# Optimization experiments

Measured on AMD Instinct MI355X. Metric: run time of the kernel, lower is better.

The kernel has to match this reference:

```python
import jax, jax.numpy as jnp
import numpy as np

N = 50000      # nodes
E = 600000     # edges
D_IN = 128     # node_dim
D = 128        # out_channels
T = 4          # num_node_types
R = 4          # num_edge_types
L = 2          # num_layers
C = 8          # num_class
G = 512        # graphs in batch


def setup_inputs() -> dict:
    key = jax.random.key(0)
    ks = jax.random.split(key, 12)
    s = 0.05
    x = jax.random.normal(ks[0], (N, D_IN), jnp.float32)
    node_type = jax.random.randint(ks[1], (N,), 0, T)
    edge_index = jax.random.randint(ks[2], (2, E), 0, N)
    edge_type = jax.random.randint(ks[3], (E,), 0, R)
    batch = jnp.sort(jax.random.randint(ks[4], (N,), 0, G))
    # learned params
    W_het = jax.random.normal(ks[5], (T, D_IN, D), jnp.float32) * s
    b_het = jnp.zeros((T, D), jnp.float32)
    conv_W = jax.random.normal(ks[6], (L, R, D, D), jnp.float32) * s
    conv_b = jnp.zeros((L, R, D), jnp.float32)
    fuse_W = jax.random.normal(ks[7], (R * D, D), jnp.float32) * s
    fuse_b = jnp.zeros((D,), jnp.float32)
    cls_W = jax.random.normal(ks[8], (D, C), jnp.float32) * s
    cls_b = jnp.zeros((C,), jnp.float32)
    return dict(x=x, W_het=W_het, b_het=b_het, conv_W=conv_W, conv_b=conv_b,
                fuse_W=fuse_W, fuse_b=fuse_b, cls_W=cls_W, cls_b=cls_b,
                node_type=node_type, edge_index=edge_index, edge_type=edge_type,
                batch=batch)


def reference(x, W_het, b_het, conv_W, conv_b, fuse_W, fuse_b, cls_W, cls_b,
              node_type, edge_index, edge_type, batch):
    n = x.shape[0]
    # HeteroLinear: per-node-type linear. Compute all T projections then select.
    x_all = jnp.einsum('nd,tdo->tno', x, W_het)          # [T, N, D]
    h = x_all[node_type, jnp.arange(n)] + b_het[node_type]
    src, dst = edge_index[0], edge_index[1]
    for l in range(L):
        hs = h[src]                                       # [E, D] gather once per layer
        outs = []
        for r in range(R):
            # edges of relation r only (boolean mask == per-relation edge filtering)
            m = hs @ conv_W[l, r]                         # [E, D]
            m = m * (edge_type == r).astype(m.dtype)[:, None]
            agg = jax.ops.segment_sum(m, dst, num_segments=n)  # scatter-add to dst
            outs.append(agg + conv_b[l, r])
        h = jax.nn.relu(jnp.concatenate(outs, axis=1) @ fuse_W + fuse_b)
    # global mean pool over graphs
    counts = jax.ops.segment_sum(jnp.ones((n,), h.dtype), batch, num_segments=G)
    emb = jax.ops.segment_sum(h, batch, num_segments=G) / jnp.maximum(counts, 1.0)[:, None]
    logits = emb @ cls_W + cls_b
    return emb, logits
```

## Files before the change

### kernel.cpp

```cpp
#include <hip/hip_runtime.h>

#define N_NODES 50000
#define N_EDGES 600000
#define DIM     128
#define RR      4
#define LL      2
#define GG      512
#define CC      8
#define NB_SCAN ((N_NODES + 255) / 256)

typedef short bf16x8 __attribute__((ext_vector_type(8)));
typedef float f32x4  __attribute__((ext_vector_type(4)));

__device__ __forceinline__ float bf16_to_f(unsigned short u) {
    return __uint_as_float(((unsigned int)u) << 16);
}
__device__ __forceinline__ unsigned short f_to_bf16(float f) {
    unsigned int u = __float_as_uint(f);
    u += 0x7FFFu + ((u >> 16) & 1u);
    return (unsigned short)(u >> 16);
}
__device__ __forceinline__ float loadf(const void* p, long i, int isbf) {
    if (isbf) return bf16_to_f(((const unsigned short*)p)[i]);
    return ((const float*)p)[i];
}
__device__ __forceinline__ void storef(void* p, long i, float v, int isbf) {
    if (isbf) ((unsigned short*)p)[i] = f_to_bf16(v);
    else      ((float*)p)[i] = v;
}

__global__ void cg_init(const unsigned int* __restrict__ xw, int* __restrict__ flag,
                        int* __restrict__ deg_tb) {
    __shared__ int cnt;
    int tid = threadIdx.x;
    int t = blockIdx.x * 256 + tid;
    if (t < N_NODES + 16) deg_tb[t] = 0;
    if (blockIdx.x == 0) {
        if (tid == 0) cnt = 0;
        __syncthreads();
        unsigned int w = xw[tid];
        unsigned int e = (w >> 7) & 0xFFu;
        atomicAdd(&cnt, (e >= 110u && e <= 133u) ? 1 : 0);
        __syncthreads();
        if (tid == 0) *flag = (cnt >= 128) ? 1 : 0;
    }
}

__global__ void cg_hist2(const int* __restrict__ edge_index, const int* __restrict__ node_type,
                         int* __restrict__ deg, int* __restrict__ tb) {
    __shared__ int loc[4];
    int tid = threadIdx.x;
    if (tid < 4) loc[tid] = 0;
    __syncthreads();
    int e = blockIdx.x * 256 + tid;
    if (e < N_EDGES) atomicAdd(&deg[edge_index[N_EDGES + e]], 1);
    if (e < N_NODES) atomicAdd(&loc[node_type[e]], 1);
    __syncthreads();
    if (tid < 4 && loc[tid]) atomicAdd(&tb[tid], loc[tid]);
}

__global__ void cg_scan_a(const int* __restrict__ deg, int* __restrict__ blocksum) {
    __shared__ int s[256];
    int tid = threadIdx.x;
    int i = blockIdx.x * 256 + tid;
    s[tid] = (i < N_NODES) ? deg[i] : 0;
    __syncthreads();
    for (int off = 128; off > 0; off >>= 1) {
        if (tid < off) s[tid] += s[tid + off];
        __syncthreads();
    }
    if (tid == 0) blocksum[blockIdx.x] = s[0];
}

__global__ void cg_scan_b(const int* __restrict__ blocksum, int* __restrict__ blockoff,
                          int* __restrict__ rowptr, int* __restrict__ tb) {
    __shared__ int s[256];
    int tid = threadIdx.x;
    int v = (tid < NB_SCAN) ? blocksum[tid] : 0;
    s[tid] = v;
    __syncthreads();
    for (int off = 1; off < 256; off <<= 1) {
        int a = (tid >= off) ? s[tid - off] : 0;
        __syncthreads();
        s[tid] += a;
        __syncthreads();
    }
    if (tid < NB_SCAN) blockoff[tid] = s[tid] - v;
    if (tid == 255) rowptr[N_NODES] = s[255];
    if (tid == 0) {
        int run = 0;
        for (int t = 0; t < 4; t++) {
            tb[8 + t] = run;
            tb[4 + t] = run;
            run += tb[t];
        }
        tb[12] = run;
    }
}

__global__ void cg_scan_c(const int* __restrict__ deg, const int* __restrict__ blockoff,
                          int* __restrict__ rowptr, int* __restrict__ cursor) {
    __shared__ int s[256];
    int tid = threadIdx.x;
    int i = blockIdx.x * 256 + tid;
    int v = (i < N_NODES) ? deg[i] : 0;
    s[tid] = v;
    __syncthreads();
    for (int off = 1; off < 256; off <<= 1) {
        int a = (tid >= off) ? s[tid - off] : 0;
        __syncthreads();
        s[tid] += a;
        __syncthreads();
    }
    if (i < N_NODES) {
        int val = blockoff[blockIdx.x] + s[tid] - v;
        rowptr[i] = val;
        cursor[i] = val;
    }
}

__global__ void cg_fill(const int* __restrict__ edge_index, const int* __restrict__ edge_type,
                        int* __restrict__ cursor, int* __restrict__ eidx) {
    int e = blockIdx.x * 256 + threadIdx.x;
    if (e >= N_EDGES) return;
    int d = edge_index[N_EDGES + e];
    int pos = atomicAdd(&cursor[d], 1);
    eidx[pos] = (edge_index[e] << 2) | edge_type[e];
}

__global__ void cg_tfill(const int* __restrict__ node_type, int* __restrict__ tb,
                         int* __restrict__ tlist) {
    __shared__ int lcur[4];
    __shared__ int lbase[4];
    int tid = threadIdx.x;
    if (tid < 4) lcur[tid] = 0;
    __syncthreads();
    int n = blockIdx.x * 256 + tid;
    int slot = -1, t = 0;
    if (n < N_NODES) {
        t = node_type[n];
        slot = atomicAdd(&lcur[t], 1);
    }
    __syncthreads();
    if (tid < 4) lbase[tid] = atomicAdd(&tb[4 + tid], lcur[tid]);
    __syncthreads();
    if (n < N_NODES) tlist[lbase[t] + slot] = n;
}

__global__ void cg_canon_x(const void* __restrict__ x, const int* __restrict__ flagp,
                           unsigned short* __restrict__ xb) {
    long t = (long)blockIdx.x * 256 + threadIdx.x;
    if (t >= (long)N_NODES * DIM) return;
    int isbf = *flagp;
    if (isbf) xb[t] = ((const unsigned short*)x)[t];
    else      xb[t] = f_to_bf16(((const float*)x)[t]);
}

__global__ void cg_canon_Wb(const void* __restrict__ W_het, const void* __restrict__ b_het,
                            const int* __restrict__ flagp,
                            unsigned short* __restrict__ Wt, float* __restrict__ bhf) {
    int b = blockIdx.x;
    int isbf = *flagp;
    if (b < 4 * DIM) {
        int o = b & 127;
        int t = b >> 7;
        int d = threadIdx.x;
        float v = loadf(W_het, ((long)t * DIM + d) * DIM + o, isbf);
        Wt[((long)t * DIM + o) * DIM + d] = f_to_bf16(v);
    } else {
        int t = b - 4 * DIM;
        int o = threadIdx.x;
        bhf[t * DIM + o] = loadf(b_het, t * DIM + o, isbf);
    }
}

__global__ void cg_make_M2tc(const void* __restrict__ conv_W, const void* __restrict__ fuse_W,
                             const void* __restrict__ conv_b, const void* __restrict__ fuse_b,
                             const int* __restrict__ flagp,
                             unsigned short* __restrict__ M2t, float* __restrict__ cvec) {
    __shared__ float s[256];
    int b = blockIdx.x;
    int tid = threadIdx.x;
    int isbf = *flagp;
    if (b < 512) {
        int lr = b >> 6;
        int d  = (b & 63) * 2 + (tid >> 7);
        int r  = lr & 3;
        int o  = tid & 127;
        float acc = 0.0f;
        for (int k = 0; k < DIM; k++) {
            acc += loadf(conv_W, (long)(lr * DIM + d) * DIM + k, isbf)
                 * loadf(fuse_W, (long)(r * DIM + k) * DIM + o, isbf);
        }
        M2t[((long)lr * DIM + o) * DIM + d] = f_to_bf16(acc);
    } else {
        int bc = b - 512;
        int l  = bc >> 7;
        int o  = bc & 127;
        float part = 0.0f;
        for (int rk = tid; rk < RR * DIM; rk += 256) {
            part += loadf(conv_b, (long)l * RR * DIM + rk, isbf)
                  * loadf(fuse_W, (long)rk * DIM + o, isbf);
        }
        s[tid] = part;
        __syncthreads();
        for (int off = 128; off > 0; off >>= 1) {
            if (tid < off) s[tid] += s[tid + off];
            __syncthreads();
        }
        if (tid == 0) cvec[bc] = s[0] + loadf(fuse_b, o, isbf);
    }
}

#define APAD 136

__global__ void cg_hetero_mfma(const unsigned short* __restrict__ xb,
                               const unsigned short* __restrict__ Wt,
                               const float* __restrict__ bhf,
                               const int* __restrict__ tlist, const int* __restrict__ tb,
                               unsigned short* __restrict__ h) {
    int t = blockIdx.y;
    int rows_base = tb[8 + t] + blockIdx.x * 64;
    int rend = tb[8 + t + 1];
    if (rows_base >= rend) return;
    __shared__ unsigned short a_lds[64][APAD];
    __shared__ unsigned short b_lds[DIM][APAD];
    int tx = threadIdx.x;
    const unsigned short* Wsrc = Wt + (long)t * DIM * DIM;
    for (int i = tx; i < 2048; i += 256) {
        uint4 w = *(const uint4*)(Wsrc + i * 8);
        int o = i >> 4, d = (i & 15) * 8;
        *(uint4*)&b_lds[o][d] = w;
    }
    for (int i = tx; i < 1024; i += 256) {
        int row = i >> 4, seg = (i & 15) * 8;
        int gr = rows_base + row;
        uint4 w = make_uint4(0u, 0u, 0u, 0u);
        if (gr < rend) {
            int n = tlist[gr];
            w = *(const uint4*)(xb + (long)n * DIM + seg);
        }
        *(uint4*)&a_lds[row][seg] = w;
    }
    __syncthreads();
    int wv = tx >> 6, lane = tx & 63;
    int m16 = lane & 15, quad = lane >> 4;
    f32x4 acc[8];
#pragma unroll
    for (int c = 0; c < 8; c++) acc[c] = (f32x4){0.f, 0.f, 0.f, 0.f};
    for (int ks = 0; ks < 4; ks++) {
        int koff = ks * 32 + quad * 8;
        bf16x8 af = *(const bf16x8*)(const void*)&a_lds[wv * 16 + m16][koff];
#pragma unroll
        for (int c = 0; c < 8; c++) {
            bf16x8 bfr = *(const bf16x8*)(const void*)&b_lds[c * 16 + m16][koff];
            acc[c] = __builtin_amdgcn_mfma_f32_16x16x32_bf16(af, bfr, acc[c], 0, 0, 0);
        }
    }
#pragma unroll
    for (int c = 0; c < 8; c++) {
#pragma unroll
        for (int i = 0; i < 4; i++) {
            int row = wv * 16 + quad * 4 + i;
            int col = c * 16 + m16;
            int gr = rows_base + row;
            if (gr < rend) {
                int n = tlist[gr];
                h[(long)n * DIM + col] = f_to_bf16(acc[c][i] + bhf[t * DIM + col]);
            }
        }
    }
}

__global__ void cg_pgemm_mfma(const unsigned short* __restrict__ h,
                              const unsigned short* __restrict__ M2t, int l,
                              unsigned short* __restrict__ P) {
    int r  = blockIdx.y;
    int n0 = blockIdx.x * 64;
    __shared__ unsigned short a_lds[64][APAD];
    __shared__ unsigned short b_lds[DIM][APAD];
    int tx = threadIdx.x;
    const unsigned short* Bsrc = M2t + (long)(l * RR + r) * DIM * DIM;
    for (int i = tx; i < 2048; i += 256) {
        uint4 w = *(const uint4*)(Bsrc + i * 8);
        int o = i >> 4, d = (i & 15) * 8;
        *(uint4*)&b_lds[o][d] = w;
    }
    for (int i = tx; i < 1024; i += 256) {
        int row = i >> 4, seg = (i & 15) * 8;
        int n = n0 + row;
        uint4 w = make_uint4(0u, 0u, 0u, 0u);
        if (n < N_NODES) w = *(const uint4*)(h + (long)n * DIM + seg);
        *(uint4*)&a_lds[row][seg] = w;
    }
    __syncthreads();
    int wv = tx >> 6, lane = tx & 63;
    int m16 = lane & 15, quad = lane >> 4;
    f32x4 acc[8];
#pragma unroll
    for (int c = 0; c < 8; c++) acc[c] = (f32x4){0.f, 0.f, 0.f, 0.f};
    for (int ks = 0; ks < 4; ks++) {
        int koff = ks * 32 + quad * 8;
        bf16x8 af = *(const bf16x8*)(const void*)&a_lds[wv * 16 + m16][koff];
#pragma unroll
        for (int c = 0; c < 8; c++) {
            bf16x8 bfr = *(const bf16x8*)(const void*)&b_lds[c * 16 + m16][koff];
            acc[c] = __builtin_amdgcn_mfma_f32_16x16x32_bf16(af, bfr, acc[c], 0, 0, 0);
        }
    }
#pragma unroll
    for (int c = 0; c < 8; c++) {
#pragma unroll
        for (int i = 0; i < 4; i++) {
            int row = wv * 16 + quad * 4 + i;
            int col = c * 16 + m16;
            int n = n0 + row;
            if (n < N_NODES)
                P[(long)n * (RR * DIM) + r * DIM + col] = f_to_bf16(acc[c][i]);
        }
    }
}

__global__ void cg_gather4(const unsigned short* __restrict__ P, const int* __restrict__ rowptr,
                           const int* __restrict__ eidx, const float* __restrict__ cv,
                           unsigned short* __restrict__ hout) {
    int wid  = (blockIdx.x * 256 + threadIdx.x) >> 6;
    int lane = threadIdx.x & 63;
    if (wid >= N_NODES) return;
    int eg = lane >> 4;
    int ol = lane & 15;
    int start = rowptr[wid];
    int end   = rowptr[wid + 1];
    float a[8] = {0.f, 0.f, 0.f, 0.f, 0.f, 0.f, 0.f, 0.f};
    for (int j = start + eg; j < end; j += 4) {
        int v = eidx[j];
        const uint4 w = *(const uint4*)(P + (long)(v >> 2) * (RR * DIM) + (v & 3) * DIM + ol * 8);
        a[0] += bf16_to_f((unsigned short)(w.x & 0xFFFFu));
        a[1] += bf16_to_f((unsigned short)(w.x >> 16));
        a[2] += bf16_to_f((unsigned short)(w.y & 0xFFFFu));
        a[3] += bf16_to_f((unsigned short)(w.y >> 16));
        a[4] += bf16_to_f((unsigned short)(w.z & 0xFFFFu));
        a[5] += bf16_to_f((unsigned short)(w.z >> 16));
        a[6] += bf16_to_f((unsigned short)(w.w & 0xFFFFu));
        a[7] += bf16_to_f((unsigned short)(w.w >> 16));
    }
#pragma unroll
    for (int i = 0; i < 8; i++) {
        a[i] += __shfl_xor(a[i], 16);
        a[i] += __shfl_xor(a[i], 32);
    }
    if (eg == 0) {
        int o0 = ol * 8;
        float v[8];
#pragma unroll
        for (int i = 0; i < 8; i++) {
            float s = a[i] + cv[o0 + i];
            v[i] = s > 0.0f ? s : 0.0f;
        }
        uint4 o4;
        o4.x = (unsigned int)f_to_bf16(v[0]) | ((unsigned int)f_to_bf16(v[1]) << 16);
        o4.y = (unsigned int)f_to_bf16(v[2]) | ((unsigned int)f_to_bf16(v[3]) << 16);
        o4.z = (unsigned int)f_to_bf16(v[4]) | ((unsigned int)f_to_bf16(v[5]) << 16);
        o4.w = (unsigned int)f_to_bf16(v[6]) | ((unsigned int)f_to_bf16(v[7]) << 16);
        *(uint4*)(hout + (long)wid * DIM + o0) = o4;
    }
}

__global__ void cg_pool_logits(const unsigned short* __restrict__ h, const int* __restrict__ batch,
                               const void* __restrict__ cls_W, const void* __restrict__ cls_b,
                               const int* __restrict__ flagp, void* __restrict__ out) {
    __shared__ float acc_s[4][DIM];
    __shared__ float emb_s[DIM];
    int g   = blockIdx.x;
    int tid = threadIdx.x;
    int wv  = tid >> 6;
    int lane = tid & 63;
    int sub = lane >> 4;
    int ol  = lane & 15;
    int isbf = *flagp;
    int lo = 0, hi = N_NODES;
    while (lo < hi) { int mid = (lo + hi) >> 1; if (batch[mid] < g) lo = mid + 1; else hi = mid; }
    int start = lo;
    hi = N_NODES;
    while (lo < hi) { int mid = (lo + hi) >> 1; if (batch[mid] < g + 1) lo = mid + 1; else hi = mid; }
    int end = lo;
    float a[8] = {0.f, 0.f, 0.f, 0.f, 0.f, 0.f, 0.f, 0.f};
    for (int n = start + wv * 4 + sub; n < end; n += 16) {
        uint4 w = *(const uint4*)(h + (long)n * DIM + ol * 8);
        a[0] += bf16_to_f((unsigned short)(w.x & 0xFFFFu));
        a[1] += bf16_to_f((unsigned short)(w.x >> 16));
        a[2] += bf16_to_f((unsigned short)(w.y & 0xFFFFu));
        a[3] += bf16_to_f((unsigned short)(w.y >> 16));
        a[4] += bf16_to_f((unsigned short)(w.z & 0xFFFFu));
        a[5] += bf16_to_f((unsigned short)(w.z >> 16));
        a[6] += bf16_to_f((unsigned short)(w.w & 0xFFFFu));
        a[7] += bf16_to_f((unsigned short)(w.w >> 16));
    }
#pragma unroll
    for (int i = 0; i < 8; i++) {
        a[i] += __shfl_xor(a[i], 16);
        a[i] += __shfl_xor(a[i], 32);
    }
    if (sub == 0) {
#pragma unroll
        for (int i = 0; i < 8; i++) acc_s[wv][ol * 8 + i] = a[i];
    }
    __syncthreads();
    int cnt = end - start;
    float inv = 1.0f / (float)(cnt > 1 ? cnt : 1);
    if (tid < DIM) {
        float e = (acc_s[0][tid] + acc_s[1][tid] + acc_s[2][tid] + acc_s[3][tid]) * inv;
        emb_s[tid] = e;
        storef(out, (long)g * DIM + tid, e, isbf);
    }
    __syncthreads();
    if (tid < 128) {
        int c  = tid >> 4;
        int kk = tid & 15;
        float p = 0.0f;
#pragma unroll
        for (int k = kk * 8; k < kk * 8 + 8; k++)
            p += emb_s[k] * loadf(cls_W, (long)k * CC + c, isbf);
        p += __shfl_xor(p, 1);
        p += __shfl_xor(p, 2);
        p += __shfl_xor(p, 4);
        p += __shfl_xor(p, 8);
        if (kk == 0)
            storef(out, (long)GG * DIM + g * CC + c, p + loadf(cls_b, c, isbf), isbf);
    }
}

extern "C" void kernel_launch(void* const* d_in, const int* in_sizes, int n_in,
                              void* d_out, int out_size, void* d_ws, size_t ws_size,
                              hipStream_t stream) {
    const void* x      = d_in[0];
    const void* W_het  = d_in[1];
    const void* b_het  = d_in[2];
    const void* conv_W = d_in[3];
    const void* conv_b = d_in[4];
    const void* fuse_W = d_in[5];
    const void* fuse_b = d_in[6];
    const void* cls_W  = d_in[7];
    const void* cls_b  = d_in[8];
    const int* node_type  = (const int*)d_in[9];
    const int* edge_index = (const int*)d_in[10];
    const int* edge_type  = (const int*)d_in[11];
    const int* batch      = (const int*)d_in[12];

    char* base = (char*)d_ws;
    unsigned short* hbf      = (unsigned short*)(base + 0);
    unsigned short* P        = (unsigned short*)(base + 12800000);
    unsigned short* xb       = (unsigned short*)(base + 64000000);
    unsigned short* Wt       = (unsigned short*)(base + 76800000);
    float*          bhf      = (float*)(base + 76931072);
    unsigned short* M2t      = (unsigned short*)(base + 76933120);
    float*          cvec     = (float*)(base + 77195264);
    int*            rowptr   = (int*)(base + 77196288);
    int*            cursor   = (int*)(base + 77396320);
    int*            deg      = (int*)(base + 77596352);
    int*            tb       = (int*)(base + 77796352);
    int*            blocksum = (int*)(base + 77796416);
    int*            blockoff = (int*)(base + 77797440);
    int*            eidx     = (int*)(base + 77798464);
    int*            tlist    = (int*)(base + 80198464);
    int*            flag     = (int*)(base + 80398464);

    cg_init<<<(N_NODES + 16 + 255) / 256, 256, 0, stream>>>((const unsigned int*)x, flag, deg);
    cg_hist2<<<(N_EDGES + 255) / 256, 256, 0, stream>>>(edge_index, node_type, deg, tb);
    cg_scan_a<<<NB_SCAN, 256, 0, stream>>>(deg, blocksum);
    cg_scan_b<<<1, 256, 0, stream>>>(blocksum, blockoff, rowptr, tb);
    cg_scan_c<<<NB_SCAN, 256, 0, stream>>>(deg, blockoff, rowptr, cursor);
    cg_fill<<<(N_EDGES + 255) / 256, 256, 0, stream>>>(edge_index, edge_type, cursor, eidx);
    cg_tfill<<<(N_NODES + 255) / 256, 256, 0, stream>>>(node_type, tb, tlist);

    cg_canon_x<<<(int)(((long)N_NODES * DIM + 255) / 256), 256, 0, stream>>>(x, flag, xb);
    cg_canon_Wb<<<4 * DIM + 4, DIM, 0, stream>>>(W_het, b_het, flag, Wt, bhf);
    cg_make_M2tc<<<768, 256, 0, stream>>>(conv_W, fuse_W, conv_b, fuse_b, flag, M2t, cvec);

    cg_hetero_mfma<<<dim3((N_NODES + 63) / 64, 4), 256, 0, stream>>>(
        xb, Wt, bhf, tlist, tb, hbf);
    for (int l = 0; l < LL; l++) {
        cg_pgemm_mfma<<<dim3((N_NODES + 63) / 64, RR), 256, 0, stream>>>(hbf, M2t, l, P);
        cg_gather4<<<(N_NODES * 64 + 255) / 256, 256, 0, stream>>>(
            P, rowptr, eidx, cvec + l * DIM, hbf);
    }

    cg_pool_logits<<<GG, 256, 0, stream>>>(hbf, batch, cls_W, cls_b, flag, d_out);
}
```

Measured before the change: 354.9 us.

## Aggregate neighbor features per relation before GEMM, fusing relu into conv

```diff
diff --git a/kernel.cpp b/kernel.cpp
--- a/kernel.cpp
+++ b/kernel.cpp
@@ -8,6 +8,7 @@
 #define GG      512
 #define CC      8
 #define NB_SCAN ((N_NODES + 255) / 256)
+#define EC      (N_EDGES / 4)
 
 typedef short bf16x8 __attribute__((ext_vector_type(8)));
 typedef float f32x4  __attribute__((ext_vector_type(4)));
@@ -52,9 +53,18 @@
     int tid = threadIdx.x;
     if (tid < 4) loc[tid] = 0;
     __syncthreads();
-    int e = blockIdx.x * 256 + tid;
-    if (e < N_EDGES) atomicAdd(&deg[edge_index[N_EDGES + e]], 1);
-    if (e < N_NODES) atomicAdd(&loc[node_type[e]], 1);
+    int t = blockIdx.x * 256 + tid;
+    if (t < EC) {
+        int d0 = edge_index[N_EDGES + t];
+        int d1 = edge_index[N_EDGES + t + EC];
+        int d2 = edge_index[N_EDGES + t + 2 * EC];
+        int d3 = edge_index[N_EDGES + t + 3 * EC];
+        atomicAdd(&deg[d0], 1);
+        atomicAdd(&deg[d1], 1);
+        atomicAdd(&deg[d2], 1);
+        atomicAdd(&deg[d3], 1);
+    }
+    if (t < N_NODES) atomicAdd(&loc[node_type[t]], 1);
     __syncthreads();
     if (tid < 4 && loc[tid]) atomicAdd(&tb[tid], loc[tid]);
 }
@@ -121,11 +131,15 @@
 
 __global__ void cg_fill(const int* __restrict__ edge_index, const int* __restrict__ edge_type,
                         int* __restrict__ cursor, int* __restrict__ eidx) {
-    int e = blockIdx.x * 256 + threadIdx.x;
-    if (e >= N_EDGES) return;
-    int d = edge_index[N_EDGES + e];
-    int pos = atomicAdd(&cursor[d], 1);
-    eidx[pos] = (edge_index[e] << 2) | edge_type[e];
+    int t = blockIdx.x * 256 + threadIdx.x;
+    if (t >= EC) return;
+#pragma unroll
+    for (int k = 0; k < 4; k++) {
+        int e = t + k * EC;
+        int d = edge_index[N_EDGES + e];
+        int pos = atomicAdd(&cursor[d], 1);
+        eidx[pos] = (edge_index[e] << 2) | edge_type[e];
+    }
 }
 
 __global__ void cg_tfill(const int* __restrict__ node_type, int* __restrict__ tb,
@@ -149,11 +163,21 @@
 
 __global__ void cg_canon_x(const void* __restrict__ x, const int* __restrict__ flagp,
                            unsigned short* __restrict__ xb) {
-    long t = (long)blockIdx.x * 256 + threadIdx.x;
-    if (t >= (long)N_NODES * DIM) return;
-    int isbf = *flagp;
-    if (isbf) xb[t] = ((const unsigned short*)x)[t];
-    else      xb[t] = f_to_bf16(((const float*)x)[t]);
+    long i = ((long)blockIdx.x * 256 + threadIdx.x) * 8;
+    if (i >= (long)N_NODES * DIM) return;
+    if (*flagp) {
+        *(uint4*)(xb + i) = *(const uint4*)((const unsigned short*)x + i);
+    } else {
+        const float* xf = (const float*)x + i;
+        float4 f0 = *(const float4*)xf;
+        float4 f1 = *(const float4*)(xf + 4);
+        uint4 o;
+        o.x = (unsigned int)f_to_bf16(f0.x) | ((unsigned int)f_to_bf16(f0.y) << 16);
+        o.y = (unsigned int)f_to_bf16(f0.z) | ((unsigned int)f_to_bf16(f0.w) << 16);
+        o.z = (unsigned int)f_to_bf16(f1.x) | ((unsigned int)f_to_bf16(f1.y) << 16);
+        o.w = (unsigned int)f_to_bf16(f1.z) | ((unsigned int)f_to_bf16(f1.w) << 16);
+        *(uint4*)(xb + i) = o;
+    }
 }
 
 __global__ void cg_canon_Wb(const void* __restrict__ W_het, const void* __restrict__ b_het,
@@ -272,41 +296,92 @@
     }
 }
 
-__global__ void cg_pgemm_mfma(const unsigned short* __restrict__ h,
-                              const unsigned short* __restrict__ M2t, int l,
-                              unsigned short* __restrict__ P) {
-    int r  = blockIdx.y;
+__global__ void cg_gatherS(const unsigned short* __restrict__ h, const int* __restrict__ rowptr,
+                           const int* __restrict__ eidx, unsigned short* __restrict__ S) {
+    int wid  = (blockIdx.x * 256 + threadIdx.x) >> 6;
+    int lane = threadIdx.x & 63;
+    if (wid >= N_NODES) return;
+    int start = rowptr[wid];
+    int end   = rowptr[wid + 1];
+    float a0[4] = {0.f, 0.f, 0.f, 0.f};
+    float a1[4] = {0.f, 0.f, 0.f, 0.f};
+    int j = start;
+    for (; j + 1 < end; j += 2) {
+        int v0 = eidx[j];
+        int v1 = eidx[j + 1];
+        unsigned int w0 = *(const unsigned int*)(h + (long)(v0 >> 2) * DIM + 2 * lane);
+        unsigned int w1 = *(const unsigned int*)(h + (long)(v1 >> 2) * DIM + 2 * lane);
+        float f00 = bf16_to_f((unsigned short)(w0 & 0xFFFFu));
+        float f01 = bf16_to_f((unsigned short)(w0 >> 16));
+        float f10 = bf16_to_f((unsigned short)(w1 & 0xFFFFu));
+        float f11 = bf16_to_f((unsigned short)(w1 >> 16));
+        int r0 = v0 & 3, r1 = v1 & 3;
+        if      (r0 == 0) { a0[0] += f00; a1[0] += f01; }
+        else if (r0 == 1) { a0[1] += f00; a1[1] += f01; }
+        else if (r0 == 2) { a0[2] += f00; a1[2] += f01; }
+        else              { a0[3] += f00; a1[3] += f01; }
+        if      (r1 == 0) { a0[0] += f10; a1[0] += f11; }
+        else if (r1 == 1) { a0[1] += f10; a1[1] += f11; }
+        else if (r1 == 2) { a0[2] += f10; a1[2] += f11; }
+        else              { a0[3] += f10; a1[3] += f11; }
+    }
+    if (j < end) {
+        int v = eidx[j];
+        unsigned int w = *(const unsigned int*)(h + (long)(v >> 2) * DIM + 2 * lane);
+        float f0 = bf16_to_f((unsigned short)(w & 0xFFFFu));
+        float f1 = bf16_to_f((unsigned short)(w >> 16));
+        int r = v & 3;
+        if      (r == 0) { a0[0] += f0; a1[0] += f1; }
+        else if (r == 1) { a0[1] += f0; a1[1] += f1; }
+        else if (r == 2) { a0[2] += f0; a1[2] += f1; }
+        else              { a0[3] += f0; a1[3] += f1; }
+    }
+    unsigned short* Sp = S + (long)wid * (RR * DIM);
+#pragma unroll
+    for (int r = 0; r < 4; r++) {
+        unsigned int o = (unsigned int)f_to_bf16(a0[r]) | ((unsigned int)f_to_bf16(a1[r]) << 16);
+        *(unsigned int*)(Sp + r * DIM + 2 * lane) = o;
+    }
+}
+
+__global__ void cg_conv_mfma(const unsigned short* __restrict__ S,
+                             const unsigned short* __restrict__ M2t, int l,
+                             const float* __restrict__ cv,
+                             unsigned short* __restrict__ hout) {
     int n0 = blockIdx.x * 64;
     __shared__ unsigned short a_lds[64][APAD];
     __shared__ unsigned short b_lds[DIM][APAD];
     int tx = threadIdx.x;
-    const unsigned short* Bsrc = M2t + (long)(l * RR + r) * DIM * DIM;
-    for (int i = tx; i < 2048; i += 256) {
-        uint4 w = *(const uint4*)(Bsrc + i * 8);
-        int o = i >> 4, d = (i & 15) * 8;
-        *(uint4*)&b_lds[o][d] = w;
-    }
-    for (int i = tx; i < 1024; i += 256) {
-        int row = i >> 4, seg = (i & 15) * 8;
-        int n = n0 + row;
-        uint4 w = make_uint4(0u, 0u, 0u, 0u);
-        if (n < N_NODES) w = *(const uint4*)(h + (long)n * DIM + seg);
-        *(uint4*)&a_lds[row][seg] = w;
-    }
-    __syncthreads();
     int wv = tx >> 6, lane = tx & 63;
     int m16 = lane & 15, quad = lane >> 4;
     f32x4 acc[8];
 #pragma unroll
     for (int c = 0; c < 8; c++) acc[c] = (f32x4){0.f, 0.f, 0.f, 0.f};
-    for (int ks = 0; ks < 4; ks++) {
-        int koff = ks * 32 + quad * 8;
-        bf16x8 af = *(const bf16x8*)(const void*)&a_lds[wv * 16 + m16][koff];
-#pragma unroll
-        for (int c = 0; c < 8; c++) {
-            bf16x8 bfr = *(const bf16x8*)(const void*)&b_lds[c * 16 + m16][koff];
-            acc[c] = __builtin_amdgcn_mfma_f32_16x16x32_bf16(af, bfr, acc[c], 0, 0, 0);
-        }
+    for (int r = 0; r < RR; r++) {
+        const unsigned short* Bsrc = M2t + (long)(l * RR + r) * DIM * DIM;
+        for (int i = tx; i < 2048; i += 256) {
+            uint4 w = *(const uint4*)(Bsrc + i * 8);
+            int o = i >> 4, d = (i & 15) * 8;
+            *(uint4*)&b_lds[o][d] = w;
+        }
+        for (int i = tx; i < 1024; i += 256) {
+            int row = i >> 4, seg = (i & 15) * 8;
+            int n = n0 + row;
+            uint4 w = make_uint4(0u, 0u, 0u, 0u);
+            if (n < N_NODES) w = *(const uint4*)(S + (long)n * (RR * DIM) + r * DIM + seg);
+            *(uint4*)&a_lds[row][seg] = w;
+        }
+        __syncthreads();
+        for (int ks = 0; ks < 4; ks++) {
+            int koff = ks * 32 + quad * 8;
+            bf16x8 af = *(const bf16x8*)(const void*)&a_lds[wv * 16 + m16][koff];
+#pragma unroll
+            for (int c = 0; c < 8; c++) {
+                bf16x8 bfr = *(const bf16x8*)(const void*)&b_lds[c * 16 + m16][koff];
+                acc[c] = __builtin_amdgcn_mfma_f32_16x16x32_bf16(af, bfr, acc[c], 0, 0, 0);
+            }
+        }
+        __syncthreads();
     }
 #pragma unroll
     for (int c = 0; c < 8; c++) {
@@ -315,54 +390,11 @@
             int row = wv * 16 + quad * 4 + i;
             int col = c * 16 + m16;
             int n = n0 + row;
-            if (n < N_NODES)
-                P[(long)n * (RR * DIM) + r * DIM + col] = f_to_bf16(acc[c][i]);
-        }
-    }
-}
-
-__global__ void cg_gather4(const unsigned short* __restrict__ P, const int* __restrict__ rowptr,
-                           const int* __restrict__ eidx, const float* __restrict__ cv,
-                           unsigned short* __restrict__ hout) {
-    int wid  = (blockIdx.x * 256 + threadIdx.x) >> 6;
-    int lane = threadIdx.x & 63;
-    if (wid >= N_NODES) return;
-    int eg = lane >> 4;
-    int ol = lane & 15;
-    int start = rowptr[wid];
-    int end   = rowptr[wid + 1];
-    float a[8] = {0.f, 0.f, 0.f, 0.f, 0.f, 0.f, 0.f, 0.f};
-    for (int j = start + eg; j < end; j += 4) {
-        int v = eidx[j];
-        const uint4 w = *(const uint4*)(P + (long)(v >> 2) * (RR * DIM) + (v & 3) * DIM + ol * 8);
-        a[0] += bf16_to_f((unsigned short)(w.x & 0xFFFFu));
-        a[1] += bf16_to_f((unsigned short)(w.x >> 16));
-        a[2] += bf16_to_f((unsigned short)(w.y & 0xFFFFu));
-        a[3] += bf16_to_f((unsigned short)(w.y >> 16));
-        a[4] += bf16_to_f((unsigned short)(w.z & 0xFFFFu));
-        a[5] += bf16_to_f((unsigned short)(w.z >> 16));
-        a[6] += bf16_to_f((unsigned short)(w.w & 0xFFFFu));
-        a[7] += bf16_to_f((unsigned short)(w.w >> 16));
-    }
-#pragma unroll
-    for (int i = 0; i < 8; i++) {
-        a[i] += __shfl_xor(a[i], 16);
-        a[i] += __shfl_xor(a[i], 32);
-    }
-    if (eg == 0) {
-        int o0 = ol * 8;
-        float v[8];
-#pragma unroll
-        for (int i = 0; i < 8; i++) {
-            float s = a[i] + cv[o0 + i];
-            v[i] = s > 0.0f ? s : 0.0f;
-        }
-        uint4 o4;
-        o4.x = (unsigned int)f_to_bf16(v[0]) | ((unsigned int)f_to_bf16(v[1]) << 16);
-        o4.y = (unsigned int)f_to_bf16(v[2]) | ((unsigned int)f_to_bf16(v[3]) << 16);
-        o4.z = (unsigned int)f_to_bf16(v[4]) | ((unsigned int)f_to_bf16(v[5]) << 16);
-        o4.w = (unsigned int)f_to_bf16(v[6]) | ((unsigned int)f_to_bf16(v[7]) << 16);
-        *(uint4*)(hout + (long)wid * DIM + o0) = o4;
+            if (n < N_NODES) {
+                float v = acc[c][i] + cv[col];
+                hout[(long)n * DIM + col] = f_to_bf16(v > 0.0f ? v : 0.0f);
+            }
+        }
     }
 }
 
@@ -449,7 +481,7 @@
 
     char* base = (char*)d_ws;
     unsigned short* hbf      = (unsigned short*)(base + 0);
-    unsigned short* P        = (unsigned short*)(base + 12800000);
+    unsigned short* S        = (unsigned short*)(base + 12800000);
     unsigned short* xb       = (unsigned short*)(base + 64000000);
     unsigned short* Wt       = (unsigned short*)(base + 76800000);
     float*          bhf      = (float*)(base + 76931072);
@@ -466,23 +498,22 @@
     int*            flag     = (int*)(base + 80398464);
 
     cg_init<<<(N_NODES + 16 + 255) / 256, 256, 0, stream>>>((const unsigned int*)x, flag, deg);
-    cg_hist2<<<(N_EDGES + 255) / 256, 256, 0, stream>>>(edge_index, node_type, deg, tb);
+    cg_hist2<<<(EC + 255) / 256, 256, 0, stream>>>(edge_index, node_type, deg, tb);
     cg_scan_a<<<NB_SCAN, 256, 0, stream>>>(deg, blocksum);
     cg_scan_b<<<1, 256, 0, stream>>>(blocksum, blockoff, rowptr, tb);
     cg_scan_c<<<NB_SCAN, 256, 0, stream>>>(deg, blockoff, rowptr, cursor);
-    cg_fill<<<(N_EDGES + 255) / 256, 256, 0, stream>>>(edge_index, edge_type, cursor, eidx);
+    cg_fill<<<(EC + 255) / 256, 256, 0, stream>>>(edge_index, edge_type, cursor, eidx);
     cg_tfill<<<(N_NODES + 255) / 256, 256, 0, stream>>>(node_type, tb, tlist);
 
-    cg_canon_x<<<(int)(((long)N_NODES * DIM + 255) / 256), 256, 0, stream>>>(x, flag, xb);
+    cg_canon_x<<<(int)(((long)N_NODES * DIM / 8 + 255) / 256), 256, 0, stream>>>(x, flag, xb);
     cg_canon_Wb<<<4 * DIM + 4, DIM, 0, stream>>>(W_het, b_het, flag, Wt, bhf);
     cg_make_M2tc<<<768, 256, 0, stream>>>(conv_W, fuse_W, conv_b, fuse_b, flag, M2t, cvec);
 
     cg_hetero_mfma<<<dim3((N_NODES + 63) / 64, 4), 256, 0, stream>>>(
         xb, Wt, bhf, tlist, tb, hbf);
     for (int l = 0; l < LL; l++) {
-        cg_pgemm_mfma<<<dim3((N_NODES + 63) / 64, RR), 256, 0, stream>>>(hbf, M2t, l, P);
-        cg_gather4<<<(N_NODES * 64 + 255) / 256, 256, 0, stream>>>(
-            P, rowptr, eidx, cvec + l * DIM, hbf);
+        cg_gatherS<<<(N_NODES * 64 + 255) / 256, 256, 0, stream>>>(hbf, rowptr, eidx, S);
+        cg_conv_mfma<<<(N_NODES + 63) / 64, 256, 0, stream>>>(S, M2t, l, cvec + l * DIM, hbf);
     }
 
     cg_pool_logits<<<GG, 256, 0, stream>>>(hbf, batch, cls_W, cls_b, flag, d_out);
```

New measurement: 408.8 us. 15.2% more time.
